# Kernel optimization log

Measured on AMD Instinct MI355X. Metric: run time of the kernel, lower is better.

## Reference

```python
import jax, jax.numpy as jnp
import numpy as np
import math

POOL = 7          # RoIAlign output_size
SR = 2            # sampling_ratio


def _roi_align(feat, boxes, bidx):
    """torchvision RoIAlign, aligned=False, spatial_scale=1.0, sampling_ratio=2.
    feat: [B,C,H,W]; boxes: [N,4] (x1,y1,x2,y2) in pixel coords of this level;
    bidx: [N] int batch indices. Returns [N,C,POOL,POOL]."""
    B, C, H, W = feat.shape
    x1, y1, x2, y2 = boxes[:, 0], boxes[:, 1], boxes[:, 2], boxes[:, 3]
    roi_w = jnp.maximum(x2 - x1, 1.0)
    roi_h = jnp.maximum(y2 - y1, 1.0)
    bin_w = roi_w / POOL
    bin_h = roi_h / POOL
    # sample-point offsets within the ROI, in bin units: [POOL, SR]
    off = jnp.arange(POOL, dtype=feat.dtype)[:, None] + (jnp.arange(SR, dtype=feat.dtype)[None, :] + 0.5) / SR
    ys = y1[:, None, None] + bin_h[:, None, None] * off  # [N,POOL,SR]
    xs = x1[:, None, None] + bin_w[:, None, None] * off  # [N,POOL,SR]

    def prep(c, size):
        valid = (c > -1.0) & (c < size)
        c = jnp.clip(c, 0.0, size - 1)
        lo = jnp.floor(c).astype(jnp.int32)
        hi = jnp.minimum(lo + 1, size - 1)
        return lo, hi, c - lo, valid

    y_lo, y_hi, fy, vy = prep(ys, H)
    x_lo, x_hi, fx, vx = prep(xs, W)

    b = bidx.astype(jnp.int32)[:, None, None, None, None]  # [N,1,1,1,1]

    def gather(yi, xi):
        # -> [N,POOL,SR,POOL,SR,C] (advanced indices broadcast, channel slice last)
        return feat[b, :, yi[:, :, :, None, None], xi[:, None, None, :, :]]

    hy = (1.0 - fy)[:, :, :, None, None, None]
    ly = fy[:, :, :, None, None, None]
    hx = (1.0 - fx)[:, None, None, :, :, None]
    lx = fx[:, None, None, :, :, None]
    v = (gather(y_lo, x_lo) * hy * hx + gather(y_lo, x_hi) * hy * lx
         + gather(y_hi, x_lo) * ly * hx + gather(y_hi, x_hi) * ly * lx)
    valid = (vy[:, :, :, None, None] & vx[:, None, None, :, :])[..., None]
    v = jnp.where(valid, v, 0.0)
    out = v.mean(axis=(2, 4))          # average over SRxSR samples -> [N,POOL,POOL,C]
    return out.transpose(0, 3, 1, 2)   # [N,C,POOL,POOL]


def setup_inputs() -> dict:
    key = jax.random.key(0)
    k2, k3, k4, k5, kxy, kwh, kbi = jax.random.split(key, 7)
    N = 1000
    p2 = jax.random.normal(k2, (2, 256, 256, 256), dtype=jnp.float32)
    p3 = jax.random.normal(k3, (2, 256, 128, 128), dtype=jnp.float32)
    p4 = jax.random.normal(k4, (2, 256, 64, 64), dtype=jnp.float32)
    p5 = jax.random.normal(k5, (2, 256, 32, 32), dtype=jnp.float32)
    xy = jax.random.uniform(kxy, (N, 2), minval=0.0, maxval=0.7)
    wh = jax.random.uniform(kwh, (N, 2), minval=0.02, maxval=0.3)
    rpn_bbox = jnp.concatenate([xy, xy + wh], axis=1)  # (x1,y1,x2,y2) normalized
    box_index = jax.random.randint(kbi, (N,), 0, 2, dtype=jnp.int32)
    return {"p2": p2, "p3": p3, "p4": p4, "p5": p5,
            "rpn_bbox": rpn_bbox, "box_index": box_index}


def reference(p2, p3, p4, p5, rpn_bbox, box_index):
    feats = [p2, p3, p4, p5]
    N = rpn_bbox.shape[0]
    x1, y1, x2, y2 = rpn_bbox[:, 0], rpn_bbox[:, 1], rpn_bbox[:, 2], rpn_bbox[:, 3]
    area = (y2 - y1) * (x2 - x1)
    roi_level = jnp.log(jnp.sqrt(area)) / math.log(2.0)
    roi_level = jnp.clip(jnp.round(roi_level) + 4.0, 0.0, 3.0).astype(jnp.int32)
    # Compute RoIAlign of every ROI at every level, then select per-ROI level.
    # (The masked-select / per-level dispatch / argsort-combine in the original
    # restores original ROI order, so this is mathematically identical.)
    pooled_per_level = jnp.stack(
        [_roi_align(f, rpn_bbox * f.shape[3], box_index) for f in feats], axis=0
    )  # [4, N, C, 7, 7]
    pooled = pooled_per_level[roi_level, jnp.arange(N)]  # [N, C, 7, 7]
    return pooled
```

## Files before the change

### kernel.cpp

```cpp
#include <hip/hip_runtime.h>
#include <math.h>

#define POOL 7
#define NCELL 49
#define NCH 256
#define CH_SPLIT 32
#define CHPB (NCH / CH_SPLIT)
#define CHPW (CHPB / 4)
#define LDSF 640
#define NIT_S 10
#define NBUCK 512

typedef __attribute__((address_space(1))) void global_void;
typedef __attribute__((address_space(3))) void lds_void;
__device__ __forceinline__ void stage4(const float* g, float* l) {
    __builtin_amdgcn_global_load_lds((global_void*)g, (lds_void*)l, 4, 0, 0);
}
__device__ __forceinline__ void stage16(const float* g, float* l) {
    __builtin_amdgcn_global_load_lds((global_void*)g, (lds_void*)l, 16, 0, 0);
}
__device__ __forceinline__ void vwait0() {
    asm volatile("s_waitcnt vmcnt(0)" ::: "memory");
}

struct BoxP {
    int W, bidx, y0, x0a, wwa, ngrp, x0, ww, packed;
    float x1, y1, bin_w, bin_h;
};

__device__ __forceinline__ BoxP compute_boxp(const float* boxes, const int* bidxp, int n)
{
    BoxP P;
    float bx1 = boxes[4 * n + 0], by1 = boxes[4 * n + 1];
    float bx2 = boxes[4 * n + 2], by2 = boxes[4 * n + 3];
    float area = (by2 - by1) * (bx2 - bx1);
    float lvlf = logf(sqrtf(area)) * 1.4426950408889634f;
    int level = (int)fminf(fmaxf(rintf(lvlf) + 4.0f, 0.0f), 3.0f);
    int W = 256 >> level;
    float scale = (float)W;
    P.W = W;
    P.bidx = bidxp[n];
    P.x1 = bx1 * scale;
    P.y1 = by1 * scale;
    P.bin_w = fmaxf((bx2 - bx1) * scale, 1.0f) * (1.0f / POOL);
    P.bin_h = fmaxf((by2 - by1) * scale, 1.0f) * (1.0f / POOL);

    float yA = P.y1 + P.bin_h * 0.25f, yB = P.y1 + P.bin_h * 6.75f;
    float xA = P.x1 + P.bin_w * 0.25f, xB = P.x1 + P.bin_w * 6.75f;
    int y0  = (int)floorf(fminf(fmaxf(yA, 0.f), (float)(W - 1)));
    int y1h = min((int)floorf(fminf(fmaxf(yB, 0.f), (float)(W - 1))) + 1, W - 1);
    int x0  = (int)floorf(fminf(fmaxf(xA, 0.f), (float)(W - 1)));
    x0 = min(x0, W - 2);
    int x1p = min((int)floorf(fminf(fmaxf(xB, 0.f), (float)(W - 1))) + 1, W - 1);
    int ww = x1p - x0 + 1;
    int wh = y1h - y0 + 1;

    int x0a = x0 & ~3;
    int wwa = ((x1p - x0a + 1) + 3) & ~3;
    if ((wwa & 7) == 0 && (wwa + 4) * wh <= LDSF) wwa += 4;
    int padded = wwa * wh;

    P.y0 = y0; P.x0 = x0; P.x0a = x0a; P.wwa = wwa; P.ww = ww;
    P.ngrp = (padded <= LDSF) ? (wwa >> 2) * wh : -1;
    int whc = min(wh, LDSF / ww);
    P.packed = ww * whc;
    return P;
}

struct TabR {
    int o0[4], o1[4];
    float w00[4], w01[4], w10[4], w11[4];
};

__device__ __forceinline__ void make_tab_arrays(
    int lane, int W, int rs, int xb, int y0,
    float x1, float y1, float bin_w, float bin_h, TabR& tb)
{
    int cell = (lane < NCELL) ? lane : (NCELL - 1);
    int py = cell / POOL, px = cell % POOL;
#pragma unroll
    for (int s = 0; s < 4; ++s) {
        int sy = s >> 1, sx = s & 1;
        float y = y1 + bin_h * ((float)py + ((float)sy + 0.5f) * 0.5f);
        float x = x1 + bin_w * ((float)px + ((float)sx + 0.5f) * 0.5f);
        bool v = (y > -1.f) && (y < (float)W) && (x > -1.f) && (x < (float)W);
        float yc = fminf(fmaxf(y, 0.f), (float)(W - 1));
        float xc = fminf(fmaxf(x, 0.f), (float)(W - 1));
        int ylo = (int)floorf(yc), xlo = (int)floorf(xc);
        int yhi = min(ylo + 1, W - 1);
        float fy = yc - (float)ylo, fx = xc - (float)xlo;
        float vv = v ? 0.25f : 0.f;
        int bxp = min(xlo, W - 2);
        bool in = (xlo == bxp);
        float wx0 = in ? (1.f - fx) : 0.f;
        float wx1 = in ? fx : 1.f;
        float wr0 = (1.f - fy) * vv, wr1 = fy * vv;
        tb.o0[s] = ((ylo - y0) * rs + (bxp - xb)) * 4;
        tb.o1[s] = ((yhi - y0) * rs + (bxp - xb)) * 4;
        tb.w00[s] = wr0 * wx0; tb.w01[s] = wr0 * wx1;
        tb.w10[s] = wr1 * wx0; tb.w11[s] = wr1 * wx1;
    }
}

__device__ __forceinline__ float consume(const float* cb, const TabR& tb)
{
    const char* b = (const char*)cb;
    float acc = 0.f;
#pragma unroll
    for (int s = 0; s < 4; ++s) {
        const float* q0 = (const float*)(b + tb.o0[s]);
        const float* q1 = (const float*)(b + tb.o1[s]);
        acc += tb.w00[s] * q0[0] + tb.w01[s] * q0[1]
             + tb.w10[s] * q1[0] + tb.w11[s] * q1[1];
    }
    return acc;
}

template <int NIT4>
__device__ __forceinline__ void box_x4(
    const float* fbase, float* outp, float* sm, int lane,
    int W, int HW, int wwa, int y0, int x0a, int ngrp, const TabR& tb)
{
    int g_off[NIT4];
    bool act[NIT4];
    int wwa4 = wwa >> 2;
#pragma unroll
    for (int k = 0; k < NIT4; ++k) {
        int idx = k * 64 + lane;
        act[k] = idx < ngrp;
        int ii = act[k] ? idx : 0;
        int r = ii / wwa4;
        int c = ii - r * wwa4;
        g_off[k] = (y0 + r) * W + x0a + c * 4;
    }
#pragma unroll
    for (int k = 0; k < NIT4; ++k)
        if (act[k]) stage16(fbase + g_off[k], sm + k * 256);
#pragma unroll
    for (int k = 0; k < NIT4; ++k)
        if (act[k]) stage16(fbase + (size_t)HW + g_off[k], sm + LDSF + k * 256);

    vwait0();
    float r0 = consume(sm, tb);
    if (lane < NCELL) outp[0] = r0;
    float r1 = consume(sm + LDSF, tb);
    if (lane < NCELL) outp[(size_t)NCELL] = r1;
}

__device__ __forceinline__ void box_s(
    const float* fbase, float* outp, float* sm, int lane,
    int W, int HW, int ww, int y0, int x0, int packed, const TabR& tb)
{
    int g_off[NIT_S];
#pragma unroll
    for (int k = 0; k < NIT_S; ++k) {
        int idx = k * 64 + lane;
        idx = (idx < packed) ? idx : 0;
        int r = idx / ww;
        int c = idx - r * ww;
        g_off[k] = (y0 + r) * W + (x0 + c);
    }
#pragma unroll
    for (int k = 0; k < NIT_S; ++k) stage4(fbase + g_off[k], sm + k * 64);
#pragma unroll
    for (int k = 0; k < NIT_S; ++k) stage4(fbase + (size_t)HW + g_off[k], sm + LDSF + k * 64);

    vwait0();
    float r0 = consume(sm, tb);
    if (lane < NCELL) outp[0] = r0;
    float r1 = consume(sm + LDSF, tb);
    if (lane < NCELL) outp[(size_t)NCELL] = r1;
}

__device__ __forceinline__ int box_key(const float* boxes, const int* bidx, int n)
{
    float bx1 = boxes[4 * n + 0], by1 = boxes[4 * n + 1];
    float bx2 = boxes[4 * n + 2], by2 = boxes[4 * n + 3];
    float area = (by2 - by1) * (bx2 - bx1);
    float lvlf = logf(sqrtf(area)) * 1.4426950408889634f;
    int level = (int)fminf(fmaxf(rintf(lvlf) + 4.0f, 0.0f), 3.0f);
    int b = bidx[n] & 1;
    float cx = 0.5f * (bx1 + bx2), cy = 0.5f * (by1 + by2);
    int qx = min(7, max(0, (int)(cx * 8.0f)));
    int qy = min(7, max(0, (int)(cy * 8.0f)));
    return (((((level << 1) | b) << 3) | qy) << 3) | qx;
}

__global__ __launch_bounds__(NBUCK) void box_sort_kernel(
    const float* __restrict__ boxes, const int* __restrict__ bidx,
    int* __restrict__ perm, int* __restrict__ prm, int N)
{
    __shared__ int h0[NBUCK], h1[NBUCK];
    const int t = threadIdx.x;
    h0[t] = 0;
    __syncthreads();
    for (int n = t; n < N; n += NBUCK)
        atomicAdd(&h0[box_key(boxes, bidx, n)], 1);
    __syncthreads();
    int* src = h0; int* dst = h1;
    for (int off = 1; off < NBUCK; off <<= 1) {
        dst[t] = src[t] + ((t >= off) ? src[t - off] : 0);
        __syncthreads();
        int* tmp = src; src = dst; dst = tmp;
    }
    dst[t] = (t == 0) ? 0 : src[t - 1];
    __syncthreads();
    for (int n = t; n < N; n += NBUCK) {
        int slot = atomicAdd(&dst[box_key(boxes, bidx, n)], 1);
        perm[slot] = n;
    }
    if (prm) {
        for (int n = t; n < N; n += NBUCK) {
            BoxP P = compute_boxp(boxes, bidx, n);
            int4* o = (int4*)(prm + (size_t)n * 16);
            o[0] = make_int4(P.W, P.bidx, P.y0, P.x0a);
            o[1] = make_int4(P.wwa, P.ngrp, P.x0, P.ww);
            o[2] = make_int4(P.packed, __float_as_int(P.x1),
                             __float_as_int(P.y1), __float_as_int(P.bin_w));
            o[3] = make_int4(__float_as_int(P.bin_h), 0, 0, 0);
        }
    }
}

__global__ __launch_bounds__(256, 8) void roi_align_fpn_kernel(
    const float* __restrict__ p2, const float* __restrict__ p3,
    const float* __restrict__ p4, const float* __restrict__ p5,
    const float* __restrict__ boxes, const int* __restrict__ bidx,
    const int* __restrict__ perm, const int* __restrict__ prm,
    float* __restrict__ out, int N)
{
    __shared__ float smem[4][CHPW][LDSF];
    const int n = perm ? perm[blockIdx.y] : (int)blockIdx.y;
    const int t = threadIdx.x;
    const int wave = t >> 6;
    const int lane = t & 63;

    BoxP P;
    if (prm) {
        const int4* ip = (const int4*)(prm + (size_t)n * 16);
        int4 q0 = ip[0], q1 = ip[1], q2 = ip[2], q3 = ip[3];
        P.W = q0.x;  P.bidx = q0.y;  P.y0 = q0.z;  P.x0a = q0.w;
        P.wwa = q1.x; P.ngrp = q1.y; P.x0 = q1.z;  P.ww = q1.w;
        P.packed = q2.x;
        P.x1 = __int_as_float(q2.y); P.y1 = __int_as_float(q2.z);
        P.bin_w = __int_as_float(q2.w); P.bin_h = __int_as_float(q3.x);
    } else {
        P = compute_boxp(boxes, bidx, n);
    }

    TabR tb;
    {
        int rs = (P.ngrp >= 0) ? P.wwa : P.ww;
        int xb = (P.ngrp >= 0) ? P.x0a : P.x0;
        make_tab_arrays(lane, P.W, rs, xb, P.y0, P.x1, P.y1, P.bin_w, P.bin_h, tb);
    }

    const int W = P.W;
    const int HW = W * W;
    const float* feat = (W == 256) ? p2 : (W == 128) ? p3 : (W == 64) ? p4 : p5;
    feat += (size_t)P.bidx * NCH * HW;

    const int ch0 = blockIdx.x * CHPB + wave * CHPW;
    const float* fbase = feat + (size_t)ch0 * HW;
    float* sm = &smem[wave][0][0];
    int cell = (lane < NCELL) ? lane : (NCELL - 1);
    float* outp = out + (size_t)n * NCH * NCELL + (size_t)ch0 * NCELL + cell;

    if (P.ngrp >= 0) {
        int nit4 = (P.ngrp + 63) >> 6;
        if (nit4 == 1)      box_x4<1>(fbase, outp, sm, lane, W, HW, P.wwa, P.y0, P.x0a, P.ngrp, tb);
        else if (nit4 == 2) box_x4<2>(fbase, outp, sm, lane, W, HW, P.wwa, P.y0, P.x0a, P.ngrp, tb);
        else                box_x4<3>(fbase, outp, sm, lane, W, HW, P.wwa, P.y0, P.x0a, P.ngrp, tb);
    } else {
        box_s(fbase, outp, sm, lane, W, HW, P.ww, P.y0, P.x0, P.packed, tb);
    }
}

extern "C" void kernel_launch(void* const* d_in, const int* in_sizes, int n_in,
                              void* d_out, int out_size, void* d_ws, size_t ws_size,
                              hipStream_t stream) {
    const float* p2    = (const float*)d_in[0];
    const float* p3    = (const float*)d_in[1];
    const float* p4    = (const float*)d_in[2];
    const float* p5    = (const float*)d_in[3];
    const float* boxes = (const float*)d_in[4];
    const int*   bidx  = (const int*)d_in[5];
    float* out = (float*)d_out;
    int N = in_sizes[5];
    int* perm = nullptr;
    int* prm  = nullptr;
    size_t permB = ((size_t)N * 4 + 15) & ~(size_t)15;
    if (d_ws && ws_size >= permB + (size_t)N * 64) {
        perm = (int*)d_ws;
        prm  = (int*)((char*)d_ws + permB);
        box_sort_kernel<<<1, NBUCK, 0, stream>>>(boxes, bidx, perm, prm, N);
    } else if (d_ws && ws_size >= (size_t)N * 4) {
        perm = (int*)d_ws;
        box_sort_kernel<<<1, NBUCK, 0, stream>>>(boxes, bidx, perm, nullptr, N);
    }
    dim3 grid(CH_SPLIT, N);
    roi_align_fpn_kernel<<<grid, 256, 0, stream>>>(p2, p3, p4, p5, boxes, bidx, perm, prm, out, N);
}
```

Measured before the change: 268.3 us.

## Share bilinear tables via LDS from one wave and pack weights as float2

Only wave 0 now builds the per-cell bilinear offset/weight table. It writes the table to LDS, and after a block barrier all four waves read it back as int4 vectors, so the table math is no longer repeated in every wave. The weights are stored as float2 pairs so the consume loop can use packed two-wide FMAs. Launch bounds drop from 8 to 6 blocks per SM. This adds a __syncthreads, extra LDS per block and possibly lower occupancy.

```diff
diff --git a/kernel.cpp b/kernel.cpp
--- a/kernel.cpp
+++ b/kernel.cpp
@@ -10,6 +10,9 @@
 #define LDSF 640
 #define NIT_S 10
 #define NBUCK 512
+#define TABDW 24
+
+typedef float f32x2 __attribute__((ext_vector_type(2)));
 
 typedef __attribute__((address_space(1))) void global_void;
 typedef __attribute__((address_space(3))) void lds_void;
@@ -67,14 +70,14 @@
     return P;
 }
 
-struct TabR {
+struct __align__(16) TabP {
     int o0[4], o1[4];
-    float w00[4], w01[4], w10[4], w11[4];
+    f32x2 w0[4], w1[4];
 };
 
-__device__ __forceinline__ void make_tab_arrays(
+__device__ __forceinline__ void make_tab(
     int lane, int W, int rs, int xb, int y0,
-    float x1, float y1, float bin_w, float bin_h, TabR& tb)
+    float x1, float y1, float bin_w, float bin_h, TabP& tb)
 {
     int cell = (lane < NCELL) ? lane : (NCELL - 1);
     int py = cell / POOL, px = cell % POOL;
@@ -97,29 +100,31 @@
         float wr0 = (1.f - fy) * vv, wr1 = fy * vv;
         tb.o0[s] = ((ylo - y0) * rs + (bxp - xb)) * 4;
         tb.o1[s] = ((yhi - y0) * rs + (bxp - xb)) * 4;
-        tb.w00[s] = wr0 * wx0; tb.w01[s] = wr0 * wx1;
-        tb.w10[s] = wr1 * wx0; tb.w11[s] = wr1 * wx1;
-    }
-}
-
-__device__ __forceinline__ float consume(const float* cb, const TabR& tb)
+        tb.w0[s] = (f32x2){wr0 * wx0, wr0 * wx1};
+        tb.w1[s] = (f32x2){wr1 * wx0, wr1 * wx1};
+    }
+}
+
+__device__ __forceinline__ float consume(const float* cb, const TabP& tb)
 {
     const char* b = (const char*)cb;
-    float acc = 0.f;
+    f32x2 acc = {0.f, 0.f};
 #pragma unroll
     for (int s = 0; s < 4; ++s) {
         const float* q0 = (const float*)(b + tb.o0[s]);
         const float* q1 = (const float*)(b + tb.o1[s]);
-        acc += tb.w00[s] * q0[0] + tb.w01[s] * q0[1]
-             + tb.w10[s] * q1[0] + tb.w11[s] * q1[1];
-    }
-    return acc;
+        f32x2 v0 = {q0[0], q0[1]};
+        f32x2 v1 = {q1[0], q1[1]};
+        acc += tb.w0[s] * v0;
+        acc += tb.w1[s] * v1;
+    }
+    return acc.x + acc.y;
 }
 
 template <int NIT4>
 __device__ __forceinline__ void box_x4(
     const float* fbase, float* outp, float* sm, int lane,
-    int W, int HW, int wwa, int y0, int x0a, int ngrp, const TabR& tb)
+    int W, int HW, int wwa, int y0, int x0a, int ngrp, const TabP& tb)
 {
     int g_off[NIT4];
     bool act[NIT4];
@@ -149,7 +154,7 @@
 
 __device__ __forceinline__ void box_s(
     const float* fbase, float* outp, float* sm, int lane,
-    int W, int HW, int ww, int y0, int x0, int packed, const TabR& tb)
+    int W, int HW, int ww, int y0, int x0, int packed, const TabP& tb)
 {
     int g_off[NIT_S];
 #pragma unroll
@@ -222,7 +227,7 @@
     }
 }
 
-__global__ __launch_bounds__(256, 8) void roi_align_fpn_kernel(
+__global__ __launch_bounds__(256, 6) void roi_align_fpn_kernel(
     const float* __restrict__ p2, const float* __restrict__ p3,
     const float* __restrict__ p4, const float* __restrict__ p5,
     const float* __restrict__ boxes, const int* __restrict__ bidx,
@@ -230,6 +235,7 @@
     float* __restrict__ out, int N)
 {
     __shared__ float smem[4][CHPW][LDSF];
+    __shared__ int tab_lds[64 * TABDW];
     const int n = perm ? perm[blockIdx.y] : (int)blockIdx.y;
     const int t = threadIdx.x;
     const int wave = t >> 6;
@@ -248,11 +254,30 @@
         P = compute_boxp(boxes, bidx, n);
     }
 
-    TabR tb;
-    {
+    if (wave == 0) {
+        TabP tb0;
         int rs = (P.ngrp >= 0) ? P.wwa : P.ww;
         int xb = (P.ngrp >= 0) ? P.x0a : P.x0;
-        make_tab_arrays(lane, P.W, rs, xb, P.y0, P.x1, P.y1, P.bin_w, P.bin_h, tb);
+        make_tab(lane, P.W, rs, xb, P.y0, P.x1, P.y1, P.bin_w, P.bin_h, tb0);
+        int4* d = (int4*)&tab_lds[lane * TABDW];
+        d[0] = *(const int4*)&tb0.o0[0];
+        d[1] = *(const int4*)&tb0.o1[0];
+        d[2] = *(const int4*)&tb0.w0[0];
+        d[3] = *(const int4*)&tb0.w0[2];
+        d[4] = *(const int4*)&tb0.w1[0];
+        d[5] = *(const int4*)&tb0.w1[2];
+    }
+    __syncthreads();
+
+    TabP tb;
+    {
+        const int4* tp = (const int4*)&tab_lds[lane * TABDW];
+        *(int4*)&tb.o0[0] = tp[0];
+        *(int4*)&tb.o1[0] = tp[1];
+        *(int4*)&tb.w0[0] = tp[2];
+        *(int4*)&tb.w0[2] = tp[3];
+        *(int4*)&tb.w1[0] = tp[4];
+        *(int4*)&tb.w1[2] = tp[5];
     }
 
     const int W = P.W;
```

Result: slower. 279.7 us (+4.2%).
